# Kernel optimization log

Hardware: AMD Instinct MI355X
Metric: run time of the kernel (lower is better)

The kernel has to match this reference:

```python
import jax, jax.numpy as jnp
import numpy as np

N = 50000      # nodes per side
E = 800000     # edges per side
G = 1024       # graphs per batch
VOCAB = 100000
EMB, GH, EH, OUT = 128, 256, 256, 128
HID = GH + EH


def setup_inputs() -> dict:
    key = jax.random.key(0)
    ks = jax.random.split(key, 32)

    def xav(k, shape):
        lim = float(np.sqrt(6.0 / (shape[0] + shape[1])))
        return jax.random.uniform(k, shape, jnp.float32, -lim, lim)

    inp = {
        "x1": jax.random.randint(ks[0], (N,), 0, 11),
        "edge_index1": jax.random.randint(ks[1], (2, E), 0, N),
        "ent1": jax.random.randint(ks[2], (G,), 0, VOCAB),
        "batch1": jnp.sort(jax.random.randint(ks[3], (N,), 0, G)),
        "x2": jax.random.randint(ks[4], (N,), 0, 11),
        "edge_index2": jax.random.randint(ks[5], (2, E), 0, N),
        "ent2": jax.random.randint(ks[6], (G,), 0, VOCAB),
        "batch2": jnp.sort(jax.random.randint(ks[7], (N,), 0, G)),
        # shared GCN params (xavier weights, zero biases as in _reset_params)
        "atom_emb": xav(ks[8], (11, EMB)),
        "gW1": xav(ks[9], (EMB, GH)), "gb1": jnp.zeros((GH,), jnp.float32),
        "gW2": xav(ks[10], (GH, GH)), "gb2": jnp.zeros((GH,), jnp.float32),
        "fcW": xav(ks[11], (GH, GH)), "fcb": jnp.zeros((GH,), jnp.float32),
        # shared entity encoder params
        "ent_emb": xav(ks[12], (VOCAB, EMB)),
        "eW1": xav(ks[13], (EMB, EH)), "eb1": jnp.zeros((EH,), jnp.float32),
        "eW2": xav(ks[14], (EH, EH)), "eb2": jnp.zeros((EH,), jnp.float32),
        # decoder params
        "dW1": xav(ks[15], (HID, HID)), "db1": jnp.zeros((HID,), jnp.float32),
        "dW2": xav(ks[16], (HID, HID)), "db2": jnp.zeros((HID,), jnp.float32),
        "dW3": xav(ks[17], (HID, OUT)), "db3": jnp.zeros((OUT,), jnp.float32),
    }
    return inp


def _gcn_conv(x, W, b, src, dst, n):
    # PyG GCNConv: self-loops + symmetric normalization, out[dst] += norm * (x@W)[src]
    h = x @ W                                   # [n, d_out]
    loop = jnp.arange(n)
    s = jnp.concatenate([src, loop])
    d = jnp.concatenate([dst, loop])
    deg = jax.ops.segment_sum(jnp.ones_like(s, h.dtype), d, num_segments=n)
    dinv = jnp.where(deg > 0, jax.lax.rsqrt(jnp.maximum(deg, 1e-12)), 0.0)
    norm = dinv[s] * dinv[d]                    # [E+n]
    out = jax.ops.segment_sum(h[s] * norm[:, None], d, num_segments=n)
    return out + b


def _gcn_branch(x, edge_index, batch, atom_emb, gW1, gb1, gW2, gb2, fcW, fcb):
    src, dst = edge_index[0], edge_index[1]
    h = atom_emb[x]                             # [N, EMB]
    h = jax.nn.relu(_gcn_conv(h, gW1, gb1, src, dst, N))
    h = jax.nn.relu(_gcn_conv(h, gW2, gb2, src, dst, N))
    # global mean pool per graph
    counts = jax.ops.segment_sum(jnp.ones((N,), h.dtype), batch, num_segments=G)
    pooled = jax.ops.segment_sum(h, batch, num_segments=G) / jnp.maximum(counts, 1.0)[:, None]
    return pooled @ fcW + fcb                   # [G, GH]


def _enc(ent, ent_emb, eW1, eb1, eW2, eb2):
    e = jax.nn.relu(ent_emb[ent])
    e = jax.nn.relu(e @ eW1 + eb1)
    return jax.nn.relu(e @ eW2 + eb2)           # [G, EH]


def reference(x1, edge_index1, ent1, batch1, x2, edge_index2, ent2, batch2,
              atom_emb, gW1, gb1, gW2, gb2, fcW, fcb,
              ent_emb, eW1, eb1, eW2, eb2,
              dW1, db1, dW2, db2, dW3, db3):
    g1 = _gcn_branch(x1, edge_index1, batch1, atom_emb, gW1, gb1, gW2, gb2, fcW, fcb)
    g2 = _gcn_branch(x2, edge_index2, batch2, atom_emb, gW1, gb1, gW2, gb2, fcW, fcb)
    e1 = _enc(ent1, ent_emb, eW1, eb1, eW2, eb2)
    e2 = _enc(ent2, ent_emb, eW1, eb1, eW2, eb2)
    eg1 = jnp.concatenate([g1, e1], axis=1)     # [G, GH+EH]
    eg2 = jnp.concatenate([g2, e2], axis=1)
    egs = jax.nn.relu(eg1 + eg2)
    h = jax.nn.relu(egs @ dW1 + db1)
    h = jax.nn.relu(h @ dW2 + db2)
    return h @ dW3 + db3                        # [G, OUT]
```

## Files before the change

### kernel.cpp

```cpp
#include <hip/hip_runtime.h>
#include <hip/hip_fp16.h>

static constexpr int kN = 50000;
static constexpr int kE = 800000;
static constexpr int kG = 1024;
static constexpr int kEMB = 128;
static constexpr int kGH = 256;
static constexpr int kEH = 256;
static constexpr int kOUT = 128;
static constexpr int kHID = 512;
static constexpr int kNB = (kN + 255) / 256;
static constexpr int kMD = 64;
static constexpr int kNBKT = 196;
static constexpr int kEPB = 3125;
static constexpr int kPBLK = 256;

typedef __attribute__((ext_vector_type(8))) _Float16 half8v;
typedef __attribute__((ext_vector_type(4))) _Float16 half4v;
typedef __attribute__((ext_vector_type(4))) float floatx4;
typedef __attribute__((ext_vector_type(2))) float floatx2;


#define HS_SCALE 128.0f
#define HS_INV   (1.0f / 128.0f)

__device__ inline void acc_fp8x4(unsigned int w, float& a0, float& a1, float& a2, float& a3) {
    floatx2 lo = __builtin_amdgcn_cvt_pk_f32_fp8(w, false);
    floatx2 hi = __builtin_amdgcn_cvt_pk_f32_fp8(w, true);
    a0 += lo[0]; a1 += lo[1]; a2 += hi[0]; a3 += hi[1];
}

__device__ inline float grp16_reduce(float v) {
    int x;
    x = __builtin_amdgcn_update_dpp(0, __float_as_int(v), 0x121, 0xF, 0xF, true);
    v += __int_as_float(x);
    x = __builtin_amdgcn_update_dpp(0, __float_as_int(v), 0x122, 0xF, 0xF, true);
    v += __int_as_float(x);
    x = __builtin_amdgcn_update_dpp(0, __float_as_int(v), 0x124, 0xF, 0xF, true);
    v += __int_as_float(x);
    x = __builtin_amdgcn_update_dpp(0, __float_as_int(v), 0x128, 0xF, 0xF, true);
    v += __int_as_float(x);
    return v;
}

__global__ void prep_kernel(const float* __restrict__ atom_emb, const float* __restrict__ gW1,
                            const float* __restrict__ gW2,
                            float* __restrict__ M11, _Float16* __restrict__ w2t,
                            _Float16* __restrict__ m11t) {
    int i = blockIdx.x * 256 + threadIdx.x;
    if (blockIdx.x < 256) {
        int k = i >> 8, n = i & 255;
        w2t[(size_t)n * kGH + k] = (_Float16)gW2[(size_t)k * kGH + n];
    } else {
        int j = i - 65536;
        if (j < 11 * kGH) {
            int r = j >> 8, c = j & 255;
            float s = 0.f;
            for (int k = 0; k < kEMB; k++) s += atom_emb[r * kEMB + k] * gW1[k * kGH + c];
            M11[j] = s;
        } else if (j < 11 * kGH + 256 * 32) {
            int j2 = j - 11 * kGH;
            int n = j2 >> 5, k = j2 & 31;
            float s = 0.f;
            if (k < 11)
                for (int p = 0; p < kEMB; p++) s += atom_emb[k * kEMB + p] * gW1[p * kGH + n];
            m11t[j2] = (_Float16)s;
        }
    }
}

__global__ void wtrans_kernel(const float* __restrict__ dW1, const float* __restrict__ dW2,
                              const float* __restrict__ dW3, const float* __restrict__ fcW,
                              const float* __restrict__ eW1, const float* __restrict__ eW2,
                              _Float16* __restrict__ dW1t, _Float16* __restrict__ dW2t,
                              _Float16* __restrict__ dW3t, _Float16* __restrict__ fcWt,
                              _Float16* __restrict__ eW1t, _Float16* __restrict__ eW2t) {
    int b = blockIdx.x;
    const float* src; _Float16* dst; int K, N, j0;
    if (b < 1024)      { src = dW1; dst = dW1t; K = 512; N = 512; j0 = b * 256; }
    else if (b < 2048) { src = dW2; dst = dW2t; K = 512; N = 512; j0 = (b - 1024) * 256; }
    else if (b < 2304) { src = dW3; dst = dW3t; K = 512; N = 128; j0 = (b - 2048) * 256; }
    else if (b < 2560) { src = fcW; dst = fcWt; K = 256; N = 256; j0 = (b - 2304) * 256; }
    else if (b < 2688) { src = eW1; dst = eW1t; K = 128; N = 256; j0 = (b - 2560) * 256; }
    else               { src = eW2; dst = eW2t; K = 256; N = 256; j0 = (b - 2688) * 256; }
    int j = j0 + threadIdx.x;
    int n = j / K, k = j - n * K;
    dst[j] = (_Float16)src[(size_t)k * N + n];
}

__global__ void gbounds_kernel(const int* __restrict__ batch1, const int* __restrict__ batch2,
                               int* __restrict__ gstart) {
    int side = blockIdx.y;
    const int* batch = side ? batch2 : batch1;
    int g = blockIdx.x * 256 + threadIdx.x;
    if (g > kG) return;
    int lo = 0, hi = kN;
    while (lo < hi) { int mid = (lo + hi) >> 1; if (batch[mid] < g) lo = mid + 1; else hi = mid; }
    gstart[side * (kG + 1) + g] = lo;
}

__global__ void binp1_kernel(const int* __restrict__ ei1, const int* __restrict__ ei2,
                             int* __restrict__ poff) {
    int side = blockIdx.y;
    const int* dst = (side ? ei2 : ei1) + kE;
    __shared__ int hist[kNBKT];
    int t = threadIdx.x;
    if (t < kNBKT) hist[t] = 0;
    __syncthreads();
    int base = blockIdx.x * kEPB;
    for (int j = t; j < kEPB; j += 256)
        atomicAdd(&hist[dst[base + j] >> 8], 1);
    __syncthreads();
    if (t < kNBKT) poff[((side * kNBKT + t) << 8) | blockIdx.x] = hist[t];
}

__global__ void scanA_kernel(int* __restrict__ poff, int* __restrict__ btot) {
    int b = blockIdx.x, side = blockIdx.y, t = threadIdx.x;
    __shared__ int s[256];
    int idx = ((side * kNBKT + b) << 8) | t;
    int v = poff[idx];
    s[t] = v;
    __syncthreads();
    for (int o = 1; o < 256; o <<= 1) {
        int u = (t >= o) ? s[t - o] : 0;
        __syncthreads();
        s[t] += u;
        __syncthreads();
    }
    poff[idx] = s[t] - v;
    if (t == 255) btot[side * kNBKT + b] = s[255];
}

__global__ void scanB_kernel(const int* __restrict__ btot, int* __restrict__ bbase) {
    int side = blockIdx.x, t = threadIdx.x;
    __shared__ int s[256];
    int v = (t < kNBKT) ? btot[side * kNBKT + t] : 0;
    s[t] = v;
    __syncthreads();
    for (int o = 1; o < 256; o <<= 1) {
        int u = (t >= o) ? s[t - o] : 0;
        __syncthreads();
        s[t] += u;
        __syncthreads();
    }
    if (t < kNBKT) bbase[side * (kNBKT + 1) + t] = s[t] - v;
    if (t == 255) bbase[side * (kNBKT + 1) + kNBKT] = s[255];
}

__launch_bounds__(256)
__global__ void binp2_kernel(const int* __restrict__ ei1, const int* __restrict__ ei2,
                             const int* __restrict__ poff, const int* __restrict__ bbase,
                             unsigned int* __restrict__ ebuf) {
    int side = blockIdx.y, blk = blockIdx.x, t = threadIdx.x;
    const int* ei = side ? ei2 : ei1;
    __shared__ int hist[kNBKT], lb[kNBKT], gb[kNBKT], scanbuf[256];
    __shared__ unsigned int sorted[kEPB];
    if (t < kNBKT) hist[t] = 0;
    __syncthreads();
    int base = blk * kEPB;
    for (int j = t; j < kEPB; j += 256)
        atomicAdd(&hist[ei[kE + base + j] >> 8], 1);
    __syncthreads();
    int v = (t < kNBKT) ? hist[t] : 0;
    scanbuf[t] = v;
    __syncthreads();
    for (int o = 1; o < 256; o <<= 1) {
        int u = (t >= o) ? scanbuf[t - o] : 0;
        __syncthreads();
        scanbuf[t] += u;
        __syncthreads();
    }
    if (t < kNBKT) {
        lb[t] = scanbuf[t] - v;
        gb[t] = bbase[side * (kNBKT + 1) + t] + poff[((side * kNBKT + t) << 8) | blk];
        hist[t] = 0;
    }
    __syncthreads();
    for (int j = t; j < kEPB; j += 256) {
        int s_ = ei[base + j];
        int d  = ei[kE + base + j];
        int b  = d >> 8;
        int r  = atomicAdd(&hist[b], 1);
        sorted[lb[b] + r] = ((unsigned int)d << 16) | (unsigned int)s_;
    }
    __syncthreads();
    for (int j = t; j < kEPB; j += 256) {
        unsigned int val = sorted[j];
        int b = val >> 24;
        int gpos = gb[b] + (j - lb[b]);
        ebuf[(size_t)side * kE + gpos] = val;
    }
}

__global__ void binp3_kernel(const unsigned int* __restrict__ ebuf, const int* __restrict__ bbase,
                             unsigned short* __restrict__ col_ell, int* __restrict__ counts,
                             float* __restrict__ dinv, int2* __restrict__ xd,
                             const int* __restrict__ x1, const int* __restrict__ x2) {
    int b = blockIdx.x, side = blockIdx.y, t = threadIdx.x;
    __shared__ int cnt[256];
    cnt[t] = 0;
    __syncthreads();
    int start = bbase[side * (kNBKT + 1) + b];
    int end   = bbase[side * (kNBKT + 1) + b + 1];
    for (int k = start + t; k < end; k += 256) {
        unsigned int v = ebuf[(size_t)side * kE + k];
        int d8 = (v >> 16) & 255;
        int slot = atomicAdd(&cnt[d8], 1);
        if (slot > kMD - 1) slot = kMD - 1;
        int node = (b << 8) | d8;
        col_ell[((size_t)side * kN + node) * kMD + slot] = (unsigned short)(v & 0xFFFFu);
    }
    __syncthreads();
    int node = (b << 8) | t;
    if (node < kN) {
        int d = cnt[t];
        counts[side * kN + node] = d;
        float dv = rsqrtf((float)(d + 1));
        dinv[side * kN + node] = dv;
        const int* x = side ? x2 : x1;
        xd[side * kN + node] = make_int2(x[node], __float_as_int(dv));
    }
}

__global__ void conv1_wt_kernel(const int2* __restrict__ xd,
                                const int* __restrict__ counts,
                                const unsigned short* __restrict__ col_ell,
                                _Float16* __restrict__ wt16) {
    int side = blockIdx.y;
    const int2* xdb = xd + (size_t)side * kN;
    const int* deg = counts + side * kN;
    const unsigned short* ci = col_ell + (size_t)side * kN * kMD;
    _Float16* wb = wt16 + (size_t)side * kN * 32;

    int tid = threadIdx.x;
    int sub = tid & 15;
    int v = blockIdx.x * 16 + (tid >> 4);

    int cnt = min(deg[v], kMD);
    const unsigned short* cv = ci + (size_t)v * kMD;
    float wt[11];
    #pragma unroll
    for (int t = 0; t < 11; t++) wt[t] = 0.f;
    for (int base = 0; base < cnt; base += 16) {
        int e = base + sub;
        int xs = 15; float ds = 0.f;
        if (e < cnt) {
            int2 t = xdb[(int)cv[e]];
            xs = t.x; ds = __int_as_float(t.y);
        }
        #pragma unroll
        for (int t = 0; t < 11; t++) wt[t] += (xs == t) ? ds : 0.f;
    }
    #pragma unroll
    for (int t = 0; t < 11; t++) wt[t] = grp16_reduce(wt[t]);

    int2 xv = xdb[v];
    float dv = __int_as_float(xv.y);
    float dv2 = dv * dv;
    float mywt = 0.f;
    #pragma unroll
    for (int t = 0; t < 11; t++) mywt = (sub == t) ? wt[t] : mywt;
    float wp = dv * mywt + dv2 * ((xv.x == sub) ? 1.f : 0.f);
    wb[(size_t)v * 32 + sub] = (_Float16)wp;
    wb[(size_t)v * 32 + 16 + sub] = (_Float16)0.f;
}

__launch_bounds__(256)
__global__ void gemm1_kernel(const _Float16* __restrict__ wt16,
                             const _Float16* __restrict__ m11t,
                             const float* __restrict__ bias,
                             _Float16* __restrict__ h2) {
    __shared__ _Float16 As[64][40];
    __shared__ _Float16 Bs[64][40];
    int side = blockIdx.z;
    const _Float16* Ab = wt16 + (size_t)side * kN * 32;
    _Float16* Ob = h2 + (size_t)side * kN * kGH;
    int tid = threadIdx.x;
    int wave = tid >> 6, lane = tid & 63;
    int quad = lane >> 4, r = lane & 15;
    int wm = wave >> 1, wn = wave & 1;
    int row0 = blockIdx.x * 64, col0 = blockIdx.y * 64;

    {
        int row = tid >> 2, seg = (tid & 3) * 8;
        int gr = row0 + row;
        if (gr >= kN) gr = kN - 1;
        *(half8v*)&As[row][seg] = *(const half8v*)(Ab + (size_t)gr * 32 + seg);
        *(half8v*)&Bs[row][seg] = *(const half8v*)(m11t + (size_t)(col0 + row) * 32 + seg);
    }
    __syncthreads();

    floatx4 acc[2][2];
    #pragma unroll
    for (int i = 0; i < 2; i++)
        #pragma unroll
        for (int j = 0; j < 2; j++) acc[i][j] = (floatx4){0.f, 0.f, 0.f, 0.f};
    half8v af[2], bf[2];
    #pragma unroll
    for (int mt = 0; mt < 2; mt++)
        af[mt] = *(const half8v*)&As[wm * 32 + mt * 16 + r][quad * 8];
    #pragma unroll
    for (int nt = 0; nt < 2; nt++)
        bf[nt] = *(const half8v*)&Bs[wn * 32 + nt * 16 + r][quad * 8];
    #pragma unroll
    for (int mt = 0; mt < 2; mt++)
        #pragma unroll
        for (int nt = 0; nt < 2; nt++)
            acc[mt][nt] = __builtin_amdgcn_mfma_f32_16x16x32_f16(af[mt], bf[nt],
                                                                 acc[mt][nt], 0, 0, 0);

    #pragma unroll
    for (int mt = 0; mt < 2; mt++) {
        #pragma unroll
        for (int i = 0; i < 4; i++) {
            int grow = row0 + wm * 32 + mt * 16 + quad * 4 + i;
            if (grow >= kN) continue;
            #pragma unroll
            for (int nt = 0; nt < 2; nt++) {
                int gcol = col0 + wn * 32 + nt * 16 + r;
                float v = acc[mt][nt][i] + bias[gcol];
                Ob[(size_t)grow * kGH + gcol] = (_Float16)fmaxf(v, 0.f);
            }
        }
    }
}

__launch_bounds__(256)
__global__ void gemm2_mfma_kernel(const _Float16* __restrict__ A,
                                  const _Float16* __restrict__ Bt,
                                  const float* __restrict__ dinv,
                                  unsigned char* __restrict__ C) {
    __shared__ _Float16 As[128][72];
    __shared__ _Float16 Bs[128][72];

    int side = blockIdx.z;
    const _Float16* Ab = A + (size_t)side * kN * kGH;
    const float* db = dinv + (size_t)side * kN;
    unsigned char* Cb = C + (size_t)side * kN * kGH;

    int tid = threadIdx.x;
    int wave = tid >> 6, lane = tid & 63;
    int quad = lane >> 4, r = lane & 15;
    int wm = wave >> 1, wn = wave & 1;
    int row0 = blockIdx.x * 128;
    int col0 = blockIdx.y * 128;

    floatx4 acc[4][4];
    #pragma unroll
    for (int i = 0; i < 4; i++)
        #pragma unroll
        for (int j = 0; j < 4; j++) acc[i][j] = (floatx4){0.f, 0.f, 0.f, 0.f};

    for (int k0 = 0; k0 < kGH; k0 += 64) {
        #pragma unroll
        for (int u = 0; u < 4; u++) {
            int idx = tid + u * 256;
            int row = idx >> 3;
            int seg = (idx & 7) * 8;
            int gr = row0 + row;
            if (gr >= kN) gr = kN - 1;
            *(half8v*)&As[row][seg] = *(const half8v*)(Ab + (size_t)gr * kGH + k0 + seg);
            *(half8v*)&Bs[row][seg] = *(const half8v*)(Bt + (size_t)(col0 + row) * kGH + k0 + seg);
        }
        __syncthreads();
        #pragma unroll
        for (int ks = 0; ks < 2; ks++) {
            half8v af[4], bf[4];
            #pragma unroll
            for (int mt = 0; mt < 4; mt++)
                af[mt] = *(const half8v*)&As[wm * 64 + mt * 16 + r][ks * 32 + quad * 8];
            #pragma unroll
            for (int nt = 0; nt < 4; nt++)
                bf[nt] = *(const half8v*)&Bs[wn * 64 + nt * 16 + r][ks * 32 + quad * 8];
            #pragma unroll
            for (int mt = 0; mt < 4; mt++)
                #pragma unroll
                for (int nt = 0; nt < 4; nt++)
                    acc[mt][nt] = __builtin_amdgcn_mfma_f32_16x16x32_f16(af[mt], bf[nt],
                                                                         acc[mt][nt], 0, 0, 0);
        }
        __syncthreads();
    }

    #pragma unroll
    for (int mt = 0; mt < 4; mt++) {
        #pragma unroll
        for (int i = 0; i < 4; i++) {
            int grow = row0 + wm * 64 + mt * 16 + quad * 4 + i;
            if (grow >= kN) continue;
            float rsq = db[grow] * HS_SCALE;
            #pragma unroll
            for (int nt = 0; nt < 4; nt++) {
                int gcol = col0 + wn * 64 + nt * 16 + r;
                float q = acc[mt][nt][i] * rsq;
                Cb[(size_t)grow * kGH + gcol] =
                    (unsigned char)__builtin_amdgcn_cvt_pk_fp8_f32(q, q, 0, false);
            }
        }
    }
}

__launch_bounds__(256)
__global__ void gemm_tail_kernel(const _Float16* __restrict__ A,
                                 const _Float16* __restrict__ Bt,
                                 void* __restrict__ Cout,
                                 int N, int K,
                                 const float* __restrict__ bias,
                                 int relu, int f32out) {
    __shared__ _Float16 As[64][72];
    __shared__ _Float16 Bs[64][72];
    int tid = threadIdx.x;
    int wave = tid >> 6, lane = tid & 63;
    int quad = lane >> 4, r = lane & 15;
    int wm = wave >> 1, wn = wave & 1;
    int row0 = blockIdx.x * 64, col0 = blockIdx.y * 64;

    floatx4 acc[2][2];
    #pragma unroll
    for (int i = 0; i < 2; i++)
        #pragma unroll
        for (int j = 0; j < 2; j++) acc[i][j] = (floatx4){0.f, 0.f, 0.f, 0.f};

    for (int k0 = 0; k0 < K; k0 += 64) {
        #pragma unroll
        for (int u = 0; u < 2; u++) {
            int idx = tid + u * 256;
            int row = idx >> 3;
            int seg = (idx & 7) * 8;
            *(half8v*)&As[row][seg] = *(const half8v*)(A + (size_t)(row0 + row) * K + k0 + seg);
            *(half8v*)&Bs[row][seg] = *(const half8v*)(Bt + (size_t)(col0 + row) * K + k0 + seg);
        }
        __syncthreads();
        #pragma unroll
        for (int ks = 0; ks < 2; ks++) {
            half8v af[2], bf[2];
            #pragma unroll
            for (int mt = 0; mt < 2; mt++)
                af[mt] = *(const half8v*)&As[wm * 32 + mt * 16 + r][ks * 32 + quad * 8];
            #pragma unroll
            for (int nt = 0; nt < 2; nt++)
                bf[nt] = *(const half8v*)&Bs[wn * 32 + nt * 16 + r][ks * 32 + quad * 8];
            #pragma unroll
            for (int mt = 0; mt < 2; mt++)
                #pragma unroll
                for (int nt = 0; nt < 2; nt++)
                    acc[mt][nt] = __builtin_amdgcn_mfma_f32_16x16x32_f16(af[mt], bf[nt],
                                                                         acc[mt][nt], 0, 0, 0);
        }
        __syncthreads();
    }

    #pragma unroll
    for (int mt = 0; mt < 2; mt++) {
        #pragma unroll
        for (int i = 0; i < 4; i++) {
            int grow = row0 + wm * 32 + mt * 16 + quad * 4 + i;
            #pragma unroll
            for (int nt = 0; nt < 2; nt++) {
                int gcol = col0 + wn * 32 + nt * 16 + r;
                float v = acc[mt][nt][i] + bias[gcol];
                if (relu) v = fmaxf(v, 0.f);
                if (f32out) ((float*)Cout)[(size_t)grow * N + gcol] = v;
                else ((_Float16*)Cout)[(size_t)grow * N + gcol] = (_Float16)v;
            }
        }
    }
}

__global__ void aggregate2_kernel(const unsigned char* __restrict__ hs, const float* __restrict__ dinv,
                                  const int* __restrict__ counts,
                                  const unsigned short* __restrict__ col_ell,
                                  const float* __restrict__ bias, _Float16* __restrict__ out) {
    int side = blockIdx.y;
    const unsigned char* hb = hs + (size_t)side * kN * kGH;
    const float* dv_ = dinv + side * kN;
    const int* deg = counts + side * kN;
    const unsigned short* ci = col_ell + (size_t)side * kN * kMD;
    _Float16* ob = out + (size_t)side * kN * kGH;

    int wave = threadIdx.x >> 6;
    int lane = threadIdx.x & 63;
    int v = blockIdx.x * 4 + wave;
    if (v >= kN) return;
    int c = lane * 4;
    float4 bia = *(const float4*)(bias + c);
    float dv = dv_[v];
    float a0 = 0.f, a1 = 0.f, a2 = 0.f, a3 = 0.f;
    acc_fp8x4(*(const unsigned int*)(hb + (size_t)v * kGH + c), a0, a1, a2, a3);
    int cnt = min(deg[v], kMD);
    int idxl = (lane < cnt) ? (int)ci[(size_t)v * kMD + lane] : 0;
    int j = 0;
    for (; j + 16 <= cnt; j += 16) {
        unsigned int w[16];
        #pragma unroll
        for (int u = 0; u < 16; u++)
            w[u] = *(const unsigned int*)(hb + (size_t)__shfl(idxl, j + u) * kGH + c);
        #pragma unroll
        for (int u = 0; u < 16; u++) acc_fp8x4(w[u], a0, a1, a2, a3);
    }
    for (; j + 8 <= cnt; j += 8) {
        unsigned int w[8];
        #pragma unroll
        for (int u = 0; u < 8; u++)
            w[u] = *(const unsigned int*)(hb + (size_t)__shfl(idxl, j + u) * kGH + c);
        #pragma unroll
        for (int u = 0; u < 8; u++) acc_fp8x4(w[u], a0, a1, a2, a3);
    }
    for (; j < cnt; j++)
        acc_fp8x4(*(const unsigned int*)(hb + (size_t)__shfl(idxl, j) * kGH + c),
                  a0, a1, a2, a3);
    float f = dv * HS_INV;
    half4v o;
    o[0] = (_Float16)fmaxf(f * a0 + bia.x, 0.f);
    o[1] = (_Float16)fmaxf(f * a1 + bia.y, 0.f);
    o[2] = (_Float16)fmaxf(f * a2 + bia.z, 0.f);
    o[3] = (_Float16)fmaxf(f * a3 + bia.w, 0.f);
    __builtin_nontemporal_store(o, (half4v*)(ob + (size_t)v * kGH + c));
}

__global__ void poolfast_kernel(const _Float16* __restrict__ h,
                                const int* __restrict__ gstart,
                                _Float16* __restrict__ pooled16) {
    int side = blockIdx.y;
    int g = blockIdx.x;
    const _Float16* hb = h + (size_t)side * kN * kGH;
    int start = gstart[side * (kG + 1) + g];
    int end   = gstart[side * (kG + 1) + g + 1];
    int wave = threadIdx.x >> 6, lane = threadIdx.x & 63;
    int c = lane * 4;
    float a0 = 0.f, a1 = 0.f, a2 = 0.f, a3 = 0.f;
    for (int v = start + wave; v < end; v += 4) {
        half4v hv = *(const half4v*)(hb + (size_t)v * kGH + c);
        a0 += (float)hv[0]; a1 += (float)hv[1];
        a2 += (float)hv[2]; a3 += (float)hv[3];
    }
    __shared__ float ps[4][256];
    *(float4*)&ps[wave][c] = make_float4(a0, a1, a2, a3);
    __syncthreads();
    int t = threadIdx.x;
    float s = ps[0][t] + ps[1][t] + ps[2][t] + ps[3][t];
    float inv = 1.0f / fmaxf((float)(end - start), 1.0f);
    pooled16[(size_t)(side * kG + g) * kGH + t] = (_Float16)(s * inv);
}

__global__ void egather_kernel(const float* __restrict__ emb,
                               const int* __restrict__ ent1, const int* __restrict__ ent2,
                               _Float16* __restrict__ e16) {
    int rr = blockIdx.x;
    int idx = (rr < kG) ? ent1[rr] : ent2[rr - kG];
    int k = threadIdx.x;
    e16[(size_t)rr * kEMB + k] = (_Float16)fmaxf(emb[(size_t)idx * kEMB + k], 0.f);
}

__global__ void egsprep_kernel(const _Float16* __restrict__ gfc16,
                               const _Float16* __restrict__ ento16,
                               _Float16* __restrict__ egs16) {
    int idx = blockIdx.x * 256 + threadIdx.x;
    int g = idx >> 6;
    int k8 = (idx & 63) * 8;
    const _Float16* src = (k8 < kGH) ? gfc16 : ento16;
    int kk = (k8 < kGH) ? k8 : k8 - kGH;
    half8v a = *(const half8v*)(src + (size_t)g * kGH + kk);
    half8v b = *(const half8v*)(src + (size_t)(g + kG) * kGH + kk);
    half8v o;
    #pragma unroll
    for (int u = 0; u < 8; u++) o[u] = (_Float16)fmaxf((float)a[u] + (float)b[u], 0.f);
    *(half8v*)(egs16 + (size_t)g * kHID + k8) = o;
}

static inline char* carve(char*& p, size_t bytes) {
    char* r = p;
    p += (bytes + 255) & ~(size_t)255;
    return r;
}

extern "C" void kernel_launch(void* const* d_in, const int* in_sizes, int n_in,
                              void* d_out, int out_size, void* d_ws, size_t ws_size,
                              hipStream_t stream) {
    const int*   x1       = (const int*)d_in[0];
    const int*   ei1      = (const int*)d_in[1];
    const int*   ent1     = (const int*)d_in[2];
    const int*   batch1   = (const int*)d_in[3];
    const int*   x2       = (const int*)d_in[4];
    const int*   ei2      = (const int*)d_in[5];
    const int*   ent2     = (const int*)d_in[6];
    const int*   batch2   = (const int*)d_in[7];
    const float* atom_emb = (const float*)d_in[8];
    const float* gW1      = (const float*)d_in[9];
    const float* gb1      = (const float*)d_in[10];
    const float* gW2      = (const float*)d_in[11];
    const float* gb2      = (const float*)d_in[12];
    const float* fcW      = (const float*)d_in[13];
    const float* fcb      = (const float*)d_in[14];
    const float* ent_emb  = (const float*)d_in[15];
    const float* eW1      = (const float*)d_in[16];
    const float* eb1      = (const float*)d_in[17];
    const float* eW2      = (const float*)d_in[18];
    const float* eb2      = (const float*)d_in[19];
    const float* dW1      = (const float*)d_in[20];
    const float* db1      = (const float*)d_in[21];
    const float* dW2      = (const float*)d_in[22];
    const float* db2      = (const float*)d_in[23];
    const float* dW3      = (const float*)d_in[24];
    const float* db3      = (const float*)d_in[25];
    float* out = (float*)d_out;

    char* p = (char*)d_ws;
    _Float16* h2_h   = (_Float16*)carve(p, (size_t)2 * kN * kGH * 2);
    unsigned char* hs8 = (unsigned char*)carve(p, (size_t)2 * kN * kGH);
    unsigned short* col_ell = (unsigned short*)carve(p, (size_t)2 * kN * kMD * 2);
    unsigned int* ebuf = (unsigned int*)carve(p, (size_t)2 * kE * 4);
    int*   poff    = (int*)  carve(p, (size_t)2 * kNBKT * 256 * 4);
    int*   btot    = (int*)  carve(p, (size_t)2 * kNBKT * 4);
    int*   bbase   = (int*)  carve(p, (size_t)2 * (kNBKT + 1) * 4);
    int*   counts  = (int*)  carve(p, (size_t)2 * kN * 4);
    float* dinv    = (float*)carve(p, (size_t)2 * kN * 4);
    int2*  xd      = (int2*) carve(p, (size_t)2 * kN * 8);
    int*   gstart  = (int*)  carve(p, (size_t)2 * (kG + 1) * 4);
    float* M11     = (float*)carve(p, 11 * kGH * 4);
    _Float16* w2t  = (_Float16*)carve(p, (size_t)kGH * kGH * 2);
    _Float16* m11t = (_Float16*)carve(p, (size_t)256 * 32 * 2);
    _Float16* wt16 = (_Float16*)carve(p, (size_t)2 * kN * 32 * 2);
    _Float16* pooled16 = (_Float16*)carve(p, (size_t)2 * kG * kGH * 2);
    _Float16* gfc16    = (_Float16*)carve(p, (size_t)2 * kG * kGH * 2);
    _Float16* e16      = (_Float16*)carve(p, (size_t)2 * kG * kEMB * 2);
    _Float16* etmp16   = (_Float16*)carve(p, (size_t)2 * kG * kEH * 2);
    _Float16* ento16   = (_Float16*)carve(p, (size_t)2 * kG * kEH * 2);
    _Float16* egs16    = (_Float16*)carve(p, (size_t)kG * kHID * 2);
    _Float16* dh1_16   = (_Float16*)carve(p, (size_t)kG * kHID * 2);
    _Float16* dh2_16   = (_Float16*)carve(p, (size_t)kG * kHID * 2);
    _Float16* dW1t = (_Float16*)carve(p, (size_t)kHID * kHID * 2);
    _Float16* dW2t = (_Float16*)carve(p, (size_t)kHID * kHID * 2);
    _Float16* dW3t = (_Float16*)carve(p, (size_t)kOUT * kHID * 2);
    _Float16* fcWt = (_Float16*)carve(p, (size_t)kGH * kGH * 2);
    _Float16* eW1t = (_Float16*)carve(p, (size_t)kEH * kEMB * 2);
    _Float16* eW2t = (_Float16*)carve(p, (size_t)kEH * kEH * 2);

    prep_kernel<<<299, 256, 0, stream>>>(atom_emb, gW1, gW2, M11, w2t, m11t);
    wtrans_kernel<<<2944, 256, 0, stream>>>(dW1, dW2, dW3, fcW, eW1, eW2,
                                            dW1t, dW2t, dW3t, fcWt, eW1t, eW2t);
    gbounds_kernel<<<dim3((kG + 256) / 256, 2), 256, 0, stream>>>(batch1, batch2, gstart);
    binp1_kernel<<<dim3(kPBLK, 2), 256, 0, stream>>>(ei1, ei2, poff);
    scanA_kernel<<<dim3(kNBKT, 2), 256, 0, stream>>>(poff, btot);
    scanB_kernel<<<2, 256, 0, stream>>>(btot, bbase);
    binp2_kernel<<<dim3(kPBLK, 2), 256, 0, stream>>>(ei1, ei2, poff, bbase, ebuf);
    binp3_kernel<<<dim3(kNBKT, 2), 256, 0, stream>>>(ebuf, bbase, col_ell, counts,
                                                     dinv, xd, x1, x2);
    conv1_wt_kernel<<<dim3(kN / 16, 2), 256, 0, stream>>>(xd, counts, col_ell, wt16);
    gemm1_kernel<<<dim3((kN + 63) / 64, kGH / 64, 2), 256, 0, stream>>>(wt16, m11t,
                                                                        gb1, h2_h);
    gemm2_mfma_kernel<<<dim3((kN + 127) / 128, kGH / 128, 2), 256, 0, stream>>>(h2_h, w2t,
                                                                                dinv, hs8);
    aggregate2_kernel<<<dim3((kN + 3) / 4, 2), 256, 0, stream>>>(hs8, dinv, counts, col_ell,
                                                                 gb2, h2_h);
    poolfast_kernel<<<dim3(kG, 2), 256, 0, stream>>>(h2_h, gstart, pooled16);
    egather_kernel<<<2 * kG, 128, 0, stream>>>(ent_emb, ent1, ent2, e16);

    gemm_tail_kernel<<<dim3(2 * kG / 64, kGH / 64), 256, 0, stream>>>(
        pooled16, fcWt, gfc16, kGH, kGH, fcb, 0, 0);
    gemm_tail_kernel<<<dim3(2 * kG / 64, kEH / 64), 256, 0, stream>>>(
        e16, eW1t, etmp16, kEH, kEMB, eb1, 1, 0);
    gemm_tail_kernel<<<dim3(2 * kG / 64, kEH / 64), 256, 0, stream>>>(
        etmp16, eW2t, ento16, kEH, kEH, eb2, 1, 0);
    egsprep_kernel<<<kG * kHID / 8 / 256, 256, 0, stream>>>(gfc16, ento16, egs16);
    gemm_tail_kernel<<<dim3(kG / 64, kHID / 64), 256, 0, stream>>>(
        egs16, dW1t, dh1_16, kHID, kHID, db1, 1, 0);
    gemm_tail_kernel<<<dim3(kG / 64, kHID / 64), 256, 0, stream>>>(
        dh1_16, dW2t, dh2_16, kHID, kHID, db2, 1, 0);
    gemm_tail_kernel<<<dim3(kG / 64, kOUT / 64), 256, 0, stream>>>(
        dh2_16, dW3t, out, kOUT, kHID, db3, 0, 1);
}
```

Measured before the change: 398.1 us.

## Fuse first GCN dense layer into second GEMM, recomputing h1 tiles in LDS

Removes the separate gemm1 kernel, which wrote the [N,256] fp16 hidden activation to global memory. That activation was then re-read by gemm2. Instead, each gemm2 block computes its A tile on the fly with one MFMA per 16x16 sub-tile from the 32-wide wt16 rows and the M11 weights, applies bias and ReLU, and writes the result straight into shared memory. This saves a kernel launch and roughly 50 MB of global write+read traffic. In exchange, the first-layer product is recomputed for each of the two column blocks (blockIdx.y).

```diff
diff --git a/kernel.cpp b/kernel.cpp
--- a/kernel.cpp
+++ b/kernel.cpp
@@ -266,75 +266,17 @@
 }
 
 __launch_bounds__(256)
-__global__ void gemm1_kernel(const _Float16* __restrict__ wt16,
-                             const _Float16* __restrict__ m11t,
-                             const float* __restrict__ bias,
-                             _Float16* __restrict__ h2) {
-    __shared__ _Float16 As[64][40];
-    __shared__ _Float16 Bs[64][40];
-    int side = blockIdx.z;
-    const _Float16* Ab = wt16 + (size_t)side * kN * 32;
-    _Float16* Ob = h2 + (size_t)side * kN * kGH;
-    int tid = threadIdx.x;
-    int wave = tid >> 6, lane = tid & 63;
-    int quad = lane >> 4, r = lane & 15;
-    int wm = wave >> 1, wn = wave & 1;
-    int row0 = blockIdx.x * 64, col0 = blockIdx.y * 64;
-
-    {
-        int row = tid >> 2, seg = (tid & 3) * 8;
-        int gr = row0 + row;
-        if (gr >= kN) gr = kN - 1;
-        *(half8v*)&As[row][seg] = *(const half8v*)(Ab + (size_t)gr * 32 + seg);
-        *(half8v*)&Bs[row][seg] = *(const half8v*)(m11t + (size_t)(col0 + row) * 32 + seg);
-    }
-    __syncthreads();
-
-    floatx4 acc[2][2];
-    #pragma unroll
-    for (int i = 0; i < 2; i++)
-        #pragma unroll
-        for (int j = 0; j < 2; j++) acc[i][j] = (floatx4){0.f, 0.f, 0.f, 0.f};
-    half8v af[2], bf[2];
-    #pragma unroll
-    for (int mt = 0; mt < 2; mt++)
-        af[mt] = *(const half8v*)&As[wm * 32 + mt * 16 + r][quad * 8];
-    #pragma unroll
-    for (int nt = 0; nt < 2; nt++)
-        bf[nt] = *(const half8v*)&Bs[wn * 32 + nt * 16 + r][quad * 8];
-    #pragma unroll
-    for (int mt = 0; mt < 2; mt++)
-        #pragma unroll
-        for (int nt = 0; nt < 2; nt++)
-            acc[mt][nt] = __builtin_amdgcn_mfma_f32_16x16x32_f16(af[mt], bf[nt],
-                                                                 acc[mt][nt], 0, 0, 0);
-
-    #pragma unroll
-    for (int mt = 0; mt < 2; mt++) {
-        #pragma unroll
-        for (int i = 0; i < 4; i++) {
-            int grow = row0 + wm * 32 + mt * 16 + quad * 4 + i;
-            if (grow >= kN) continue;
-            #pragma unroll
-            for (int nt = 0; nt < 2; nt++) {
-                int gcol = col0 + wn * 32 + nt * 16 + r;
-                float v = acc[mt][nt][i] + bias[gcol];
-                Ob[(size_t)grow * kGH + gcol] = (_Float16)fmaxf(v, 0.f);
-            }
-        }
-    }
-}
-
-__launch_bounds__(256)
-__global__ void gemm2_mfma_kernel(const _Float16* __restrict__ A,
-                                  const _Float16* __restrict__ Bt,
-                                  const float* __restrict__ dinv,
-                                  unsigned char* __restrict__ C) {
+__global__ void gemm2f_kernel(const _Float16* __restrict__ wt16,
+                              const _Float16* __restrict__ m11t,
+                              const float* __restrict__ b1,
+                              const _Float16* __restrict__ Bt,
+                              const float* __restrict__ dinv,
+                              unsigned char* __restrict__ C) {
     __shared__ _Float16 As[128][72];
     __shared__ _Float16 Bs[128][72];
 
     int side = blockIdx.z;
-    const _Float16* Ab = A + (size_t)side * kN * kGH;
+    const _Float16* Aw = wt16 + (size_t)side * kN * 32;
     const float* db = dinv + (size_t)side * kN;
     unsigned char* Cb = C + (size_t)side * kN * kGH;
 
@@ -351,16 +293,37 @@
         #pragma unroll
         for (int j = 0; j < 4; j++) acc[i][j] = (floatx4){0.f, 0.f, 0.f, 0.f};
 
+    half8v afw[2];
+    #pragma unroll
+    for (int mt = 0; mt < 2; mt++) {
+        int gr = row0 + wave * 32 + mt * 16 + r;
+        if (gr >= kN) gr = kN - 1;
+        afw[mt] = *(const half8v*)(Aw + (size_t)gr * 32 + quad * 8);
+    }
+
     for (int k0 = 0; k0 < kGH; k0 += 64) {
         #pragma unroll
         for (int u = 0; u < 4; u++) {
             int idx = tid + u * 256;
             int row = idx >> 3;
             int seg = (idx & 7) * 8;
-            int gr = row0 + row;
-            if (gr >= kN) gr = kN - 1;
-            *(half8v*)&As[row][seg] = *(const half8v*)(Ab + (size_t)gr * kGH + k0 + seg);
             *(half8v*)&Bs[row][seg] = *(const half8v*)(Bt + (size_t)(col0 + row) * kGH + k0 + seg);
+        }
+        #pragma unroll
+        for (int nt = 0; nt < 4; nt++) {
+            half8v bfw = *(const half8v*)(m11t + (size_t)(k0 + nt * 16 + r) * 32 + quad * 8);
+            float4 bia = *(const float4*)(b1 + k0 + nt * 16 + quad * 4);
+            #pragma unroll
+            for (int mt = 0; mt < 2; mt++) {
+                floatx4 d = (floatx4){0.f, 0.f, 0.f, 0.f};
+                d = __builtin_amdgcn_mfma_f32_16x16x32_f16(bfw, afw[mt], d, 0, 0, 0);
+                half4v o;
+                o[0] = (_Float16)fmaxf(d[0] + bia.x, 0.f);
+                o[1] = (_Float16)fmaxf(d[1] + bia.y, 0.f);
+                o[2] = (_Float16)fmaxf(d[2] + bia.z, 0.f);
+                o[3] = (_Float16)fmaxf(d[3] + bia.w, 0.f);
+                *(half4v*)&As[wave * 32 + mt * 16 + r][nt * 16 + quad * 4] = o;
+            }
         }
         __syncthreads();
         #pragma unroll
@@ -606,7 +569,7 @@
     float* out = (float*)d_out;
 
     char* p = (char*)d_ws;
-    _Float16* h2_h   = (_Float16*)carve(p, (size_t)2 * kN * kGH * 2);
+    _Float16* h4_h   = (_Float16*)carve(p, (size_t)2 * kN * kGH * 2);
     unsigned char* hs8 = (unsigned char*)carve(p, (size_t)2 * kN * kGH);
     unsigned short* col_ell = (unsigned short*)carve(p, (size_t)2 * kN * kMD * 2);
     unsigned int* ebuf = (unsigned int*)carve(p, (size_t)2 * kE * 4);
@@ -647,13 +610,11 @@
     binp3_kernel<<<dim3(kNBKT, 2), 256, 0, stream>>>(ebuf, bbase, col_ell, counts,
                                                      dinv, xd, x1, x2);
     conv1_wt_kernel<<<dim3(kN / 16, 2), 256, 0, stream>>>(xd, counts, col_ell, wt16);
-    gemm1_kernel<<<dim3((kN + 63) / 64, kGH / 64, 2), 256, 0, stream>>>(wt16, m11t,
-                                                                        gb1, h2_h);
-    gemm2_mfma_kernel<<<dim3((kN + 127) / 128, kGH / 128, 2), 256, 0, stream>>>(h2_h, w2t,
-                                                                                dinv, hs8);
+    gemm2f_kernel<<<dim3((kN + 127) / 128, kGH / 128, 2), 256, 0, stream>>>(
+        wt16, m11t, gb1, w2t, dinv, hs8);
     aggregate2_kernel<<<dim3((kN + 3) / 4, 2), 256, 0, stream>>>(hs8, dinv, counts, col_ell,
-                                                                 gb2, h2_h);
-    poolfast_kernel<<<dim3(kG, 2), 256, 0, stream>>>(h2_h, gstart, pooled16);
+                                                                 gb2, h4_h);
+    poolfast_kernel<<<dim3(kG, 2), 256, 0, stream>>>(h4_h, gstart, pooled16);
     egather_kernel<<<2 * kG, 128, 0, stream>>>(ent_emb, ent1, ent2, e16);
 
     gemm_tail_kernel<<<dim3(2 * kG / 64, kGH / 64), 256, 0, stream>>>(
```

Measured after the change: 395.1 us. About the same (-0.8%).
